# Kernel optimization log

Measured on AMD Instinct MI355X. Metric: run time of the kernel, lower is better.

The kernel has to match this reference:

```python
import jax, jax.numpy as jnp
import numpy as np

N = 512      # HiPPO state size
L = 65536    # sequence length
DT = 1e-3    # discretization step
UNROLL = 32  # scan unroll (source uses 128; 32 keeps CPU compile fast, same math)


def _make_hippo(n_state):
    # HiPPO-LegS continuous-time (A, B), as in make_hippo
    n = np.arange(n_state)
    P = np.sqrt(1 + 2 * n)
    A = P[:, None] * P[None, :]
    A = np.tril(A) - np.diag(n)
    B = np.sqrt(2 * n + 1.0)[:, None]
    return -A, B


def _discretize(A, B, step):
    # Bilinear (Tustin) discretization, as in discretize
    I = np.eye(A.shape[0])
    BL = np.linalg.inv(I - step / 2 * A)
    Ab = BL @ (I + step / 2 * A)
    Bb = (BL * step) @ B
    return Ab, Bb


def setup_inputs() -> dict:
    key = jax.random.key(0)
    A, B = _make_hippo(N)            # float64 numpy for stable inverse
    Ab, Bb = _discretize(A, B, DT)
    u = jax.random.normal(key, (L,), dtype=jnp.float32)
    return {
        "u": u,
        "Ab": jnp.asarray(Ab, dtype=jnp.float32),   # [N, N]
        "Bb": jnp.asarray(Bb, dtype=jnp.float32),   # [N, 1]
        "x0": jnp.zeros((N,), dtype=jnp.float32),   # last_x initial state
    }


def reference(u, Ab, Bb, x0):
    # Faithful HiPPO.encode: x_{k+1} = Ab @ x_k + Bb @ u_k, returning the
    # full state trajectory f of shape [L, N] (the scan's stacked outputs).
    b = Bb[:, 0]  # Bb @ u[k, None] == b * u_k

    def step(x, u_k):
        x1 = Ab @ x + b * u_k
        return x1, x1

    _, f = jax.lax.scan(step, x0, u, unroll=UNROLL)
    return f
```

## Files before the change

### kernel.cpp

```cpp
#include <hip/hip_runtime.h>
#include <cstdint>
#include <cstddef>


typedef _Float16 half_t;
typedef _Float16 f16x8 __attribute__((ext_vector_type(8)));
typedef float f32x4 __attribute__((ext_vector_type(4)));

static constexpr int KPAD = 544;
static constexpr size_t MSZ = (size_t)512 * 512;
static constexpr float INV2048 = 1.f / 2048.f;

__device__ inline void split1(float v, half_t& h, half_t& l) {
  h = (half_t)v;
  l = (half_t)((v - (float)h) * 2048.f);
}
__device__ inline void split1r(float v, half_t& h, half_t& l) {
  h = (half_t)v;
  l = (half_t)(v - (float)h);
}

__global__ void init_kernel(float4* __restrict__ zp, const float* __restrict__ Ab,
                            float* __restrict__ V0, const float* __restrict__ x0,
                            half_t* __restrict__ xh) {
  int bid = blockIdx.x, tid = threadIdx.x;
  if (bid < 6656) {
    zp[bid * 256 + tid] = make_float4(0.f, 0.f, 0.f, 0.f);
  } else if (bid < 7680) {
    int i = (bid - 6656) * 256 + tid;
    V0[i] = Ab[i];
  } else {
    xh[tid] = (half_t)x0[tid];
    xh[tid + 256] = (half_t)x0[tid + 256];
  }
}

__global__ void kbuild_kernel(const float* __restrict__ V, const float* __restrict__ b,
                              float* __restrict__ K) {
  int gw = blockIdx.x * 4 + (threadIdx.x >> 6);
  int lane = threadIdx.x & 63;
  int t = gw >> 9, n = gw & 511;
  if (t == 0) { if (lane == 0) K[n] = b[n]; return; }
  const float* row = V + (size_t)(t - 1) * MSZ + (size_t)n * 512;
  float acc = 0.f;
#pragma unroll
  for (int m = 0; m < 512; m += 64) acc += row[m + lane] * b[m + lane];
#pragma unroll
  for (int s = 32; s; s >>= 1) acc += __shfl_down(acc, s, 64);
  if (lane == 0) K[t * 512 + n] = acc;
}

__global__ void wcat_fill_kernel(const float* __restrict__ V, const float* __restrict__ K,
                                 half_t* __restrict__ Wh, half_t* __restrict__ Wl) {
  size_t idx = (size_t)blockIdx.x * 256 + threadIdx.x;
  if (idx >= (size_t)8192 * KPAD) return;
  int row = (int)(idx / KPAD), k = (int)(idx % KPAD);
  int i = row >> 9, n = row & 511;
  float v = 0.f;
  if (k < 512) v = V[(size_t)i * MSZ + (size_t)n * 512 + k];
  else if (k < 528) { int j = k - 512; if (j <= i) v = K[(i - j) * 512 + n]; }
  half_t h, l; split1r(v, h, l);
  Wh[idx] = h; Wl[idx] = l;
}

__global__ void leaf_kernel(const float* __restrict__ u, const float* __restrict__ K,
                            half_t* __restrict__ Z) {
  __shared__ float us[16];
  int c = blockIdx.x, n = threadIdx.x;
  if (n < 16) us[n] = u[c * 16 + n];
  __syncthreads();
  float acc = 0.f;
#pragma unroll
  for (int j = 0; j < 16; ++j) acc += K[(15 - j) * 512 + n] * us[j];
  Z[(size_t)c * 512 + n] = (half_t)acc;
}

__global__ void xtail_kernel(const float* __restrict__ u,
                             half_t* __restrict__ Xh, half_t* __restrict__ Xl) {
  int idx = blockIdx.x * 256 + threadIdx.x;
  int c = idx >> 5, j = idx & 31;
  float v = (j < 16) ? u[c * 16 + j] : 0.f;
  size_t o = (size_t)c * KPAD + 512 + j;
  half_t h, l; split1r(v, h, l);
  Xh[o] = h; Xl[o] = l;
}

__device__ __forceinline__ void sq_body(
    const float* __restrict__ A, const float* __restrict__ B, float* __restrict__ C,
    int bx, int by, int sl,
    half_t* __restrict__ Ash, half_t* __restrict__ Asl,
    half_t* __restrict__ Bsh, half_t* __restrict__ Bsl) {
  int m0 = bx * 64, n0 = by * 64;
  int tid = threadIdx.x, wave = tid >> 6, lane = tid & 63;
  int wm = (wave & 1) * 32, wn = (wave >> 1) * 32;
  f32x4 acc[2][2], accc[2][2];
#pragma unroll
  for (int i = 0; i < 2; ++i)
#pragma unroll
    for (int j = 0; j < 2; ++j) {
      acc[i][j] = (f32x4){0.f, 0.f, 0.f, 0.f};
      accc[i][j] = (f32x4){0.f, 0.f, 0.f, 0.f};
    }
  int rb = tid >> 6, mm = tid & 15, kseg = (tid >> 4) & 3;
  const float* ar = A + (size_t)(m0 + rb * 16 + mm) * 512 + sl * 128 + kseg * 8;
  const float* bc = B + (size_t)(sl * 128 + kseg * 8) * 512 + n0 + rb * 16 + mm;
  float4 a0 = *(const float4*)ar, a1 = *(const float4*)(ar + 4);
  float bv[8];
#pragma unroll
  for (int j = 0; j < 8; ++j) bv[j] = bc[(size_t)j * 512];
#pragma unroll
  for (int kt = 0; kt < 4; ++kt) {
    {
      float aa[8] = {a0.x, a0.y, a0.z, a0.w, a1.x, a1.y, a1.z, a1.w};
      f16x8 hv, lv;
#pragma unroll
      for (int j = 0; j < 8; ++j) { half_t h, l; split1(aa[j], h, l); hv[j] = h; lv[j] = l; }
      *(f16x8*)(Ash + tid * 8) = hv;
      *(f16x8*)(Asl + tid * 8) = lv;
#pragma unroll
      for (int j = 0; j < 8; ++j) { half_t h, l; split1(bv[j], h, l); hv[j] = h; lv[j] = l; }
      *(f16x8*)(Bsh + tid * 8) = hv;
      *(f16x8*)(Bsl + tid * 8) = lv;
    }
    __syncthreads();
    if (kt < 3) {
      a0 = *(const float4*)(ar + (kt + 1) * 32);
      a1 = *(const float4*)(ar + (kt + 1) * 32 + 4);
#pragma unroll
      for (int j = 0; j < 8; ++j) bv[j] = bc[(size_t)((kt + 1) * 32 + j) * 512];
    }
    f16x8 afh[2], afl[2], bfh[2], bfl[2];
#pragma unroll
    for (int i = 0; i < 2; ++i) {
      int ra = (wm >> 4) + i, rbn = (wn >> 4) + i;
      afh[i] = *(const f16x8*)(Ash + ra * 512 + lane * 8);
      afl[i] = *(const f16x8*)(Asl + ra * 512 + lane * 8);
      bfh[i] = *(const f16x8*)(Bsh + rbn * 512 + lane * 8);
      bfl[i] = *(const f16x8*)(Bsl + rbn * 512 + lane * 8);
    }
#pragma unroll
    for (int i = 0; i < 2; ++i)
#pragma unroll
      for (int j = 0; j < 2; ++j) {
        acc[i][j] = __builtin_amdgcn_mfma_f32_16x16x32_f16(afh[i], bfh[j], acc[i][j], 0, 0, 0);
        accc[i][j] = __builtin_amdgcn_mfma_f32_16x16x32_f16(afh[i], bfl[j], accc[i][j], 0, 0, 0);
        accc[i][j] = __builtin_amdgcn_mfma_f32_16x16x32_f16(afl[i], bfh[j], accc[i][j], 0, 0, 0);
      }
    __syncthreads();
  }
  int ml = lane & 15, quad = lane >> 4;
  for (int i = 0; i < 2; ++i)
    for (int j = 0; j < 2; ++j)
      for (int rr = 0; rr < 4; ++rr) {
        int gm = m0 + wm + i * 16 + quad * 4 + rr;
        int gn = n0 + wn + j * 16 + ml;
        atomicAdd(&C[(size_t)gm * 512 + gn], acc[i][j][rr] + accc[i][j][rr] * INV2048);
      }
}

__global__ __launch_bounds__(256)
void gemm_nn512(const float* __restrict__ A, long sA,
                const float* __restrict__ B, long sB,
                float* __restrict__ C, long sC) {
  __shared__ __align__(16) half_t s0[64 * 32], s1[64 * 32], s2[64 * 32], s3[64 * 32];
  int bz = blockIdx.z, bb = bz >> 2, sl = bz & 3;
  sq_body(A + (size_t)bb * sA, B + (size_t)bb * sB, C + (size_t)bb * sC,
          blockIdx.x, blockIdx.y, sl, s0, s1, s2, s3);
}

__device__ __forceinline__ void sweep_body(
    const half_t* __restrict__ A, long ldA, const float* __restrict__ BT,
    const half_t* __restrict__ D, long ldD,
    half_t* __restrict__ Ch, half_t* __restrict__ Cl, long ldC,
    int rScale, int rOff, int doCopy, int M, int bx, int by,
    half_t* __restrict__ Ash, half_t* __restrict__ Bsh, half_t* __restrict__ Bsl) {
  int m0 = bx * 64, n0 = by * 64;
  int tid = threadIdx.x, wave = tid >> 6, lane = tid & 63;
  int wm = (wave & 1) * 32, wn = (wave >> 1) * 32;
  f32x4 acc[2][2], accc[2][2];
#pragma unroll
  for (int i = 0; i < 2; ++i)
#pragma unroll
    for (int j = 0; j < 2; ++j) {
      acc[i][j] = (f32x4){0.f, 0.f, 0.f, 0.f};
      accc[i][j] = (f32x4){0.f, 0.f, 0.f, 0.f};
    }
  int rb = tid >> 6, mm = tid & 15, kseg = (tid >> 4) & 3;
  int arow = m0 + rb * 16 + mm;
  const half_t* ap = A + (size_t)arow * ldA + kseg * 8;
  const float* bp = BT + (size_t)(n0 + rb * 16 + mm) * 512 + kseg * 8;
  f16x8 av = (f16x8){0, 0, 0, 0, 0, 0, 0, 0};
  if (arow < M) av = *(const f16x8*)ap;
  float4 bv0 = *(const float4*)bp;
  float4 bv1 = *(const float4*)(bp + 4);
#pragma unroll
  for (int kt = 0; kt < 16; ++kt) {
    int k0 = kt * 32;
    *(f16x8*)(Ash + tid * 8) = av;
    if (doCopy && k0 >= n0 && k0 < n0 + 64 && arow < M) {
      size_t co = (size_t)(2 * arow) * ldC + k0 + kseg * 8;
      *(f16x8*)(Ch + co) = av;
      if (Cl) *(f16x8*)(Cl + co) = (f16x8){0, 0, 0, 0, 0, 0, 0, 0};
    }
    {
      float bb[8] = {bv0.x, bv0.y, bv0.z, bv0.w, bv1.x, bv1.y, bv1.z, bv1.w};
      f16x8 hv, lv;
#pragma unroll
      for (int j = 0; j < 8; ++j) { half_t h, l; split1(bb[j], h, l); hv[j] = h; lv[j] = l; }
      *(f16x8*)(Bsh + tid * 8) = hv;
      *(f16x8*)(Bsl + tid * 8) = lv;
    }
    __syncthreads();
    if (kt < 15) {
      if (arow < M) av = *(const f16x8*)(ap + (kt + 1) * 32);
      bv0 = *(const float4*)(bp + (kt + 1) * 32);
      bv1 = *(const float4*)(bp + (kt + 1) * 32 + 4);
    }
    f16x8 af[2], bfh[2], bfl[2];
#pragma unroll
    for (int i = 0; i < 2; ++i) {
      af[i] = *(const f16x8*)(Ash + ((wm >> 4) + i) * 512 + lane * 8);
      bfh[i] = *(const f16x8*)(Bsh + ((wn >> 4) + i) * 512 + lane * 8);
      bfl[i] = *(const f16x8*)(Bsl + ((wn >> 4) + i) * 512 + lane * 8);
    }
#pragma unroll
    for (int i = 0; i < 2; ++i)
#pragma unroll
      for (int j = 0; j < 2; ++j) {
        acc[i][j] = __builtin_amdgcn_mfma_f32_16x16x32_f16(af[i], bfh[j], acc[i][j], 0, 0, 0);
        accc[i][j] = __builtin_amdgcn_mfma_f32_16x16x32_f16(af[i], bfl[j], accc[i][j], 0, 0, 0);
      }
    __syncthreads();
  }
  int ml = lane & 15, quad = lane >> 4;
  for (int i = 0; i < 2; ++i)
    for (int j = 0; j < 2; ++j)
      for (int rr = 0; rr < 4; ++rr) {
        int gm = m0 + wm + i * 16 + quad * 4 + rr;
        int gn = n0 + wn + j * 16 + ml;
        if (gm >= M) continue;
        float v = acc[i][j][rr] + accc[i][j][rr] * INV2048;
        if (D) v += (float)D[(size_t)gm * ldD + gn];
        size_t co = ((size_t)gm * rScale + rOff) * ldC + gn;
        if (Cl) { half_t h, l; split1r(v, h, l); Ch[co] = h; Cl[co] = l; }
        else Ch[co] = (half_t)v;
      }
}

__global__ __launch_bounds__(256)
void gemm_nt_sweep(const half_t* __restrict__ A, long ldA,
                   const float* __restrict__ BT,
                   const half_t* __restrict__ D, long ldD,
                   half_t* __restrict__ Ch, half_t* __restrict__ Cl,
                   long ldC, int rScale, int rOff, int doCopy, int M) {
  __shared__ __align__(16) half_t s0[64 * 32], s1[64 * 32], s2[64 * 32];
  sweep_body(A, ldA, BT, D, ldD, Ch, Cl, ldC, rScale, rOff, doCopy, M,
             blockIdx.x, blockIdx.y, s0, s1, s2);
}

__global__ __launch_bounds__(256)
void fused_up(const float* __restrict__ T, float* __restrict__ Tout,
              const half_t* __restrict__ Zin, half_t* __restrict__ Zout, int M) {
  __shared__ __align__(16) half_t s0[64 * 32], s1[64 * 32], s2[64 * 32], s3[64 * 32];
  int bid = blockIdx.x;
  if (bid < 256) {
    sq_body(T, T, Tout, bid & 7, (bid >> 3) & 7, bid >> 6, s0, s1, s2, s3);
  } else {
    int b = bid - 256;
    sweep_body(Zin, 1024L, T, Zin + 512, 1024L, Zout, (half_t*)0, 512L,
               1, 0, 0, M, b >> 3, b & 7, s0, s1, s2);
  }
}

__device__ inline void load_lds16(const half_t* g, half_t* l) {
  __builtin_amdgcn_global_load_lds(
      (const __attribute__((address_space(1))) uint32_t*)g,
      (__attribute__((address_space(3))) uint32_t*)l, 16, 0, 0);
}

__global__ __launch_bounds__(512, 2)
void gemm_main(const half_t* __restrict__ Ah, const half_t* __restrict__ Al,
               const half_t* __restrict__ Bh, const half_t* __restrict__ Bl,
               float* __restrict__ C) {
  __shared__ __align__(16) half_t sm[2 * 4 * 8192];
  int bid = blockIdx.x;
  int xcd = bid & 7, loc = bid >> 3;
  int mt = (xcd & 1) * 8 + (loc >> 3);
  int nt = (xcd >> 1) * 8 + (loc & 7);
  int m0 = mt * 256, n0 = nt * 256;
  int tid = threadIdx.x, wave = tid >> 6, lane = tid & 63;
  int wm = (wave & 1) * 128, wn = (wave >> 1) * 64;
  int mm = lane & 15, kseg = lane >> 4;
  f32x4 acc[8][4];
#pragma unroll
  for (int f = 0; f < 8; ++f)
#pragma unroll
    for (int g = 0; g < 4; ++g) acc[f][g] = (f32x4){0.f, 0.f, 0.f, 0.f};

  const size_t ga0 = (size_t)(m0 + wave * 16 + mm) * KPAD + kseg * 8;
  const size_t gb0 = (size_t)(n0 + wave * 16 + mm) * KPAD + kseg * 8;
  const size_t qstep = (size_t)128 * KPAD;

  auto stage = [&](int nb, int kt, int q) {
    size_t go = (size_t)kt * 32 + (size_t)q * qstep;
    half_t* d = sm + (size_t)nb * 32768 + (size_t)(wave + 8 * q) * 512;
    load_lds16(Ah + ga0 + go, d);
    load_lds16(Al + ga0 + go, d + 8192);
    load_lds16(Bh + gb0 + go, d + 16384);
    load_lds16(Bl + gb0 + go, d + 24576);
  };

  stage(0, 0, 0);
  stage(0, 0, 1);
  asm volatile("s_waitcnt vmcnt(0)" ::: "memory");
  __builtin_amdgcn_s_barrier();

  const int lread = lane * 8;
  const int arow = (wm >> 4);
  const int brow = (wn >> 4);
  for (int kt = 0; kt < 17; ++kt) {
    const int cur = kt & 1;
    const half_t* SA_h = sm + cur * 32768;
    const half_t* SA_l = SA_h + 8192;
    const half_t* SB_h = SA_h + 16384;
    const half_t* SB_l = SA_h + 24576;
    const bool pre = kt < 16;
    f16x8 ah[4], al[4], bh0[2], bl0[2], bh1[2], bl1[2];

#pragma unroll
    for (int i = 0; i < 4; ++i) {
      ah[i] = *(const f16x8*)(SA_h + (arow + i) * 512 + lread);
      al[i] = *(const f16x8*)(SA_l + (arow + i) * 512 + lread);
    }
#pragma unroll
    for (int j = 0; j < 2; ++j) {
      bh0[j] = *(const f16x8*)(SB_h + (brow + j) * 512 + lread);
      bl0[j] = *(const f16x8*)(SB_l + (brow + j) * 512 + lread);
    }
    if (pre) stage(cur ^ 1, kt + 1, 0);
    __builtin_amdgcn_s_barrier();
    asm volatile("s_waitcnt lgkmcnt(0)" ::: "memory");
    __builtin_amdgcn_sched_barrier(0);
    __builtin_amdgcn_s_setprio(1);
#pragma unroll
    for (int i = 0; i < 4; ++i)
#pragma unroll
      for (int j = 0; j < 2; ++j) {
        acc[i][j] = __builtin_amdgcn_mfma_f32_16x16x32_f16(ah[i], bh0[j], acc[i][j], 0, 0, 0);
        acc[i][j] = __builtin_amdgcn_mfma_f32_16x16x32_f16(ah[i], bl0[j], acc[i][j], 0, 0, 0);
        acc[i][j] = __builtin_amdgcn_mfma_f32_16x16x32_f16(al[i], bh0[j], acc[i][j], 0, 0, 0);
      }
    __builtin_amdgcn_s_setprio(0);
    __builtin_amdgcn_s_barrier();

#pragma unroll
    for (int j = 0; j < 2; ++j) {
      bh1[j] = *(const f16x8*)(SB_h + (brow + 2 + j) * 512 + lread);
      bl1[j] = *(const f16x8*)(SB_l + (brow + 2 + j) * 512 + lread);
    }
    if (pre) stage(cur ^ 1, kt + 1, 1);
    __builtin_amdgcn_s_barrier();
    asm volatile("s_waitcnt lgkmcnt(0)" ::: "memory");
    __builtin_amdgcn_sched_barrier(0);
    __builtin_amdgcn_s_setprio(1);
#pragma unroll
    for (int i = 0; i < 4; ++i)
#pragma unroll
      for (int j = 0; j < 2; ++j) {
        acc[i][2 + j] = __builtin_amdgcn_mfma_f32_16x16x32_f16(ah[i], bh1[j], acc[i][2 + j], 0, 0, 0);
        acc[i][2 + j] = __builtin_amdgcn_mfma_f32_16x16x32_f16(ah[i], bl1[j], acc[i][2 + j], 0, 0, 0);
        acc[i][2 + j] = __builtin_amdgcn_mfma_f32_16x16x32_f16(al[i], bh1[j], acc[i][2 + j], 0, 0, 0);
      }
    __builtin_amdgcn_s_setprio(0);
    __builtin_amdgcn_s_barrier();

#pragma unroll
    for (int i = 0; i < 4; ++i) {
      ah[i] = *(const f16x8*)(SA_h + (arow + 4 + i) * 512 + lread);
      al[i] = *(const f16x8*)(SA_l + (arow + 4 + i) * 512 + lread);
    }
    __builtin_amdgcn_s_barrier();
    asm volatile("s_waitcnt lgkmcnt(0)" ::: "memory");
    __builtin_amdgcn_sched_barrier(0);
    __builtin_amdgcn_s_setprio(1);
#pragma unroll
    for (int i = 0; i < 4; ++i)
#pragma unroll
      for (int j = 0; j < 2; ++j) {
        acc[4 + i][2 + j] = __builtin_amdgcn_mfma_f32_16x16x32_f16(ah[i], bh1[j], acc[4 + i][2 + j], 0, 0, 0);
        acc[4 + i][2 + j] = __builtin_amdgcn_mfma_f32_16x16x32_f16(ah[i], bl1[j], acc[4 + i][2 + j], 0, 0, 0);
        acc[4 + i][2 + j] = __builtin_amdgcn_mfma_f32_16x16x32_f16(al[i], bh1[j], acc[4 + i][2 + j], 0, 0, 0);
      }
#pragma unroll
    for (int i = 0; i < 4; ++i)
#pragma unroll
      for (int j = 0; j < 2; ++j) {
        acc[4 + i][j] = __builtin_amdgcn_mfma_f32_16x16x32_f16(ah[i], bh0[j], acc[4 + i][j], 0, 0, 0);
        acc[4 + i][j] = __builtin_amdgcn_mfma_f32_16x16x32_f16(ah[i], bl0[j], acc[4 + i][j], 0, 0, 0);
        acc[4 + i][j] = __builtin_amdgcn_mfma_f32_16x16x32_f16(al[i], bh0[j], acc[4 + i][j], 0, 0, 0);
      }
    __builtin_amdgcn_s_setprio(0);
    asm volatile("s_waitcnt vmcnt(0)" ::: "memory");
    __builtin_amdgcn_s_barrier();
  }

  int ml = lane & 15, quad = lane >> 4;
#pragma unroll
  for (int f = 0; f < 8; ++f)
#pragma unroll
    for (int g = 0; g < 4; ++g) {
      int gm = m0 + wm + f * 16 + quad * 4;
      int gn = n0 + wn + g * 16 + ml;
      float* o = C + (size_t)gm * 8192 + gn;
#pragma unroll
      for (int rr = 0; rr < 4; ++rr)
        o[(size_t)rr * 8192] = acc[f][g][rr];
    }
}


extern "C" void kernel_launch(void* const* d_in, const int* in_sizes, int n_in,
                              void* d_out, int out_size, void* d_ws, size_t ws_size,
                              hipStream_t stream) {
  (void)in_sizes; (void)n_in; (void)out_size; (void)ws_size;
  const float* u  = (const float*)d_in[0];
  const float* Ab = (const float*)d_in[1];
  const float* Bb = (const float*)d_in[2];
  const float* x0 = (const float*)d_in[3];
  float* out = (float*)d_out;

  char* base = (char*)d_ws;
  size_t off = 0;
  auto carve = [&](size_t bytes) -> char* {
    char* p = base + off;
    off = (off + bytes + 255) & ~(size_t)255;
    return p;
  };
  float*  Vp  = (float*)carve(16 * MSZ * 4);
  float*  Sp  = (float*)carve(11 * MSZ * 4);
  float*  Kb  = (float*)carve((size_t)16 * 512 * 4);
  half_t* Wh  = (half_t*)carve((size_t)8192 * KPAD * 2);
  half_t* Wl  = (half_t*)carve((size_t)8192 * KPAD * 2);
  half_t* x0h = (half_t*)carve(512 * 2);
  size_t zoff[13]; zoff[0] = 0;
  for (int l = 0; l < 12; ++l) zoff[l + 1] = zoff[l] + (size_t)(4096 >> l) * 512;
  size_t xoff[13]; xoff[1] = 0;
  for (int l = 1; l < 12; ++l) xoff[l + 1] = xoff[l] + (size_t)(4096 >> l) * 512;
  half_t* Zh  = (half_t*)Vp;
  half_t* Xph = (half_t*)((char*)Vp + ((zoff[12] * 2 + 255) & ~(size_t)255));
  half_t* Xch = (half_t*)Sp;
  half_t* Xcl = (half_t*)((char*)Sp + (((size_t)4096 * KPAD * 2 + 255) & ~(size_t)255));

  hipLaunchKernelGGL(init_kernel, dim3(7681), dim3(256), 0, stream,
                     (float4*)(Vp + MSZ), Ab, Vp, x0, x0h);

  for (int s = 1; s <= 8; s <<= 1) {
    hipLaunchKernelGGL(gemm_nn512, dim3(8, 8, 4 * s), dim3(256), 0, stream,
                       Vp, (long)MSZ,
                       Vp + (size_t)(s - 1) * MSZ, 0L,
                       Vp + (size_t)s * MSZ, (long)MSZ);
  }

  hipLaunchKernelGGL(kbuild_kernel, dim3(2048), dim3(256), 0, stream, Vp, Bb, Kb);
  hipLaunchKernelGGL(wcat_fill_kernel,
                     dim3((unsigned)(((size_t)8192 * KPAD + 255) / 256)), dim3(256), 0, stream,
                     Vp, Kb, Wh, Wl);
  hipLaunchKernelGGL(leaf_kernel, dim3(4096), dim3(512), 0, stream, u, Kb, Zh);

  auto Smat = [&](int l) -> const float* {
    return (l == 0) ? (Vp + 15 * MSZ) : (Sp + (size_t)(l - 1) * MSZ);
  };

  for (int l = 1; l <= 11; ++l) {
    const float* T = (l == 1) ? Vp + 15 * MSZ : Sp + (size_t)(l - 2) * MSZ;
    float* Tout = Sp + (size_t)(l - 1) * MSZ;
    int Mup = 1 << (12 - l);
    int nswp = ((Mup + 63) / 64) * 8;
    hipLaunchKernelGGL(fused_up, dim3(256 + nswp), dim3(256), 0, stream,
                       T, Tout, Zh + zoff[l - 1], Zh + zoff[l], Mup);
  }

  for (int l = 11; l >= 0; --l) {
    int M = 1 << (11 - l);
    const half_t* Xup = (l == 11) ? x0h : Xph + xoff[l + 1];
    half_t* Ch = (l == 0) ? Xch : Xph + xoff[l];
    half_t* Cl = (l == 0) ? Xcl : (half_t*)0;
    long ldC = (l == 0) ? (long)KPAD : 512L;
    if (l == 0) {
      hipLaunchKernelGGL(xtail_kernel, dim3(512), dim3(256), 0, stream, u, Xch, Xcl);
    }
    hipLaunchKernelGGL(gemm_nt_sweep, dim3((unsigned)((M + 63) / 64), 8), dim3(256), 0, stream,
                       Xup, 512L, Smat(l),
                       Zh + zoff[l], 1024L,
                       Ch, Cl, ldC, 2, 1, 1, M);
  }

  hipLaunchKernelGGL(gemm_main, dim3(512), dim3(512), 0, stream, Xch, Xcl, Wh, Wl, out);
}
```

Baseline: 699.0 us.

## Pair down-sweep levels with precomputed product matrices to halve launches

Replaces the twelve serial down-sweep launches with six paired launches. Each launch computes two tree levels directly from the grandparent state, using a precomputed product matrix P of two adjacent level transition matrices and a precomputed Y-Z correction term. A prep kernel builds the first P and the Y-Z terms and copies one S matrix. Each pair launch also computes the next P, and the final launch absorbs the xtail work. The wcat fill is vectorised to eight elements per thread. The aim is to shorten the serial chain of small latency-bound launches. In exchange the code does extra GEMM work for the P products and has more complex indexing.

```diff
diff --git a/kernel.cpp b/kernel.cpp
--- a/kernel.cpp
+++ b/kernel.cpp
@@ -19,6 +19,166 @@
   h = (half_t)v;
   l = (half_t)(v - (float)h);
 }
+
+template <int NKT, bool ATOM>
+__device__ __forceinline__ void sq_body(
+    const float* __restrict__ A, const float* __restrict__ B, float* __restrict__ C,
+    int bx, int by, int k0off,
+    half_t* __restrict__ Ash, half_t* __restrict__ Asl,
+    half_t* __restrict__ Bsh, half_t* __restrict__ Bsl) {
+  int m0 = bx * 64, n0 = by * 64;
+  int tid = threadIdx.x, wave = tid >> 6, lane = tid & 63;
+  int wm = (wave & 1) * 32, wn = (wave >> 1) * 32;
+  f32x4 acc[2][2], accc[2][2];
+#pragma unroll
+  for (int i = 0; i < 2; ++i)
+#pragma unroll
+    for (int j = 0; j < 2; ++j) {
+      acc[i][j] = (f32x4){0.f, 0.f, 0.f, 0.f};
+      accc[i][j] = (f32x4){0.f, 0.f, 0.f, 0.f};
+    }
+  int rb = tid >> 6, mm = tid & 15, kseg = (tid >> 4) & 3;
+  const float* ar = A + (size_t)(m0 + rb * 16 + mm) * 512 + k0off + kseg * 8;
+  const float* bc = B + (size_t)(k0off + kseg * 8) * 512 + n0 + rb * 16 + mm;
+  float4 a0 = *(const float4*)ar, a1 = *(const float4*)(ar + 4);
+  float bv[8];
+#pragma unroll
+  for (int j = 0; j < 8; ++j) bv[j] = bc[(size_t)j * 512];
+#pragma unroll
+  for (int kt = 0; kt < NKT; ++kt) {
+    {
+      float aa[8] = {a0.x, a0.y, a0.z, a0.w, a1.x, a1.y, a1.z, a1.w};
+      f16x8 hv, lv;
+#pragma unroll
+      for (int j = 0; j < 8; ++j) { half_t h, l; split1(aa[j], h, l); hv[j] = h; lv[j] = l; }
+      *(f16x8*)(Ash + tid * 8) = hv;
+      *(f16x8*)(Asl + tid * 8) = lv;
+#pragma unroll
+      for (int j = 0; j < 8; ++j) { half_t h, l; split1(bv[j], h, l); hv[j] = h; lv[j] = l; }
+      *(f16x8*)(Bsh + tid * 8) = hv;
+      *(f16x8*)(Bsl + tid * 8) = lv;
+    }
+    __syncthreads();
+    if (kt < NKT - 1) {
+      a0 = *(const float4*)(ar + (kt + 1) * 32);
+      a1 = *(const float4*)(ar + (kt + 1) * 32 + 4);
+#pragma unroll
+      for (int j = 0; j < 8; ++j) bv[j] = bc[(size_t)((kt + 1) * 32 + j) * 512];
+    }
+    f16x8 afh[2], afl[2], bfh[2], bfl[2];
+#pragma unroll
+    for (int i = 0; i < 2; ++i) {
+      int ra = (wm >> 4) + i, rbn = (wn >> 4) + i;
+      afh[i] = *(const f16x8*)(Ash + ra * 512 + lane * 8);
+      afl[i] = *(const f16x8*)(Asl + ra * 512 + lane * 8);
+      bfh[i] = *(const f16x8*)(Bsh + rbn * 512 + lane * 8);
+      bfl[i] = *(const f16x8*)(Bsl + rbn * 512 + lane * 8);
+    }
+#pragma unroll
+    for (int i = 0; i < 2; ++i)
+#pragma unroll
+      for (int j = 0; j < 2; ++j) {
+        acc[i][j] = __builtin_amdgcn_mfma_f32_16x16x32_f16(afh[i], bfh[j], acc[i][j], 0, 0, 0);
+        accc[i][j] = __builtin_amdgcn_mfma_f32_16x16x32_f16(afh[i], bfl[j], accc[i][j], 0, 0, 0);
+        accc[i][j] = __builtin_amdgcn_mfma_f32_16x16x32_f16(afl[i], bfh[j], accc[i][j], 0, 0, 0);
+      }
+    __syncthreads();
+  }
+  int ml = lane & 15, quad = lane >> 4;
+  for (int i = 0; i < 2; ++i)
+    for (int j = 0; j < 2; ++j)
+      for (int rr = 0; rr < 4; ++rr) {
+        int gm = m0 + wm + i * 16 + quad * 4 + rr;
+        int gn = n0 + wn + j * 16 + ml;
+        float v = acc[i][j][rr] + accc[i][j][rr] * INV2048;
+        if (ATOM) atomicAdd(&C[(size_t)gm * 512 + gn], v);
+        else C[(size_t)gm * 512 + gn] = v;
+      }
+}
+
+__device__ __forceinline__ void sweep_body(
+    const half_t* __restrict__ A, long ldA, const float* __restrict__ BT,
+    const half_t* __restrict__ D, long ldD,
+    half_t* __restrict__ Ch, half_t* __restrict__ Cl, long ldC,
+    int rScale, int rOff, int doCopy, int M, int bx, int by,
+    half_t* __restrict__ Ash, half_t* __restrict__ Bsh, half_t* __restrict__ Bsl) {
+  int m0 = bx * 64, n0 = by * 64;
+  int tid = threadIdx.x, wave = tid >> 6, lane = tid & 63;
+  int wm = (wave & 1) * 32, wn = (wave >> 1) * 32;
+  f32x4 acc[2][2], accc[2][2];
+#pragma unroll
+  for (int i = 0; i < 2; ++i)
+#pragma unroll
+    for (int j = 0; j < 2; ++j) {
+      acc[i][j] = (f32x4){0.f, 0.f, 0.f, 0.f};
+      accc[i][j] = (f32x4){0.f, 0.f, 0.f, 0.f};
+    }
+  int rb = tid >> 6, mm = tid & 15, kseg = (tid >> 4) & 3;
+  int arow = m0 + rb * 16 + mm;
+  const half_t* ap = A + (size_t)arow * ldA + kseg * 8;
+  const float* bp = BT + (size_t)(n0 + rb * 16 + mm) * 512 + kseg * 8;
+  f16x8 av = (f16x8){0, 0, 0, 0, 0, 0, 0, 0};
+  if (arow < M) av = *(const f16x8*)ap;
+  float4 bv0 = *(const float4*)bp;
+  float4 bv1 = *(const float4*)(bp + 4);
+#pragma unroll
+  for (int kt = 0; kt < 16; ++kt) {
+    int k0 = kt * 32;
+    *(f16x8*)(Ash + tid * 8) = av;
+    if (doCopy && k0 >= n0 && k0 < n0 + 64 && arow < M) {
+      size_t co = (size_t)rScale * arow * ldC + k0 + kseg * 8;
+      *(f16x8*)(Ch + co) = av;
+      if (Cl) *(f16x8*)(Cl + co) = (f16x8){0, 0, 0, 0, 0, 0, 0, 0};
+    }
+    {
+      float bb[8] = {bv0.x, bv0.y, bv0.z, bv0.w, bv1.x, bv1.y, bv1.z, bv1.w};
+      f16x8 hv, lv;
+#pragma unroll
+      for (int j = 0; j < 8; ++j) { half_t h, l; split1(bb[j], h, l); hv[j] = h; lv[j] = l; }
+      *(f16x8*)(Bsh + tid * 8) = hv;
+      *(f16x8*)(Bsl + tid * 8) = lv;
+    }
+    __syncthreads();
+    if (kt < 15) {
+      if (arow < M) av = *(const f16x8*)(ap + (kt + 1) * 32);
+      bv0 = *(const float4*)(bp + (kt + 1) * 32);
+      bv1 = *(const float4*)(bp + (kt + 1) * 32 + 4);
+    }
+    f16x8 af[2], bfh[2], bfl[2];
+#pragma unroll
+    for (int i = 0; i < 2; ++i) {
+      af[i] = *(const f16x8*)(Ash + ((wm >> 4) + i) * 512 + lane * 8);
+      bfh[i] = *(const f16x8*)(Bsh + ((wn >> 4) + i) * 512 + lane * 8);
+      bfl[i] = *(const f16x8*)(Bsl + ((wn >> 4) + i) * 512 + lane * 8);
+    }
+#pragma unroll
+    for (int i = 0; i < 2; ++i)
+#pragma unroll
+      for (int j = 0; j < 2; ++j) {
+        acc[i][j] = __builtin_amdgcn_mfma_f32_16x16x32_f16(af[i], bfh[j], acc[i][j], 0, 0, 0);
+        accc[i][j] = __builtin_amdgcn_mfma_f32_16x16x32_f16(af[i], bfl[j], accc[i][j], 0, 0, 0);
+      }
+    __syncthreads();
+  }
+  int ml = lane & 15, quad = lane >> 4;
+  for (int i = 0; i < 2; ++i)
+    for (int j = 0; j < 2; ++j)
+      for (int rr = 0; rr < 4; ++rr) {
+        int gm = m0 + wm + i * 16 + quad * 4 + rr;
+        int gn = n0 + wn + j * 16 + ml;
+        if (gm >= M) continue;
+        float v = acc[i][j][rr] + accc[i][j][rr] * INV2048;
+        if (D) v += (float)D[(size_t)gm * ldD + gn];
+        size_t co = ((size_t)gm * rScale + rOff) * ldC + gn;
+        if (Cl) { half_t h, l; split1r(v, h, l); Ch[co] = h; Cl[co] = l; }
+        else Ch[co] = (half_t)v;
+      }
+}
+
+__device__ __forceinline__ size_t zoff_f(int l) {
+  return ((size_t)1 << 22) - ((size_t)1 << (22 - l));
+}
+
 
 __global__ void init_kernel(float4* __restrict__ zp, const float* __restrict__ Ab,
                             float* __restrict__ V0, const float* __restrict__ x0,
@@ -52,15 +212,29 @@
 
 __global__ void wcat_fill_kernel(const float* __restrict__ V, const float* __restrict__ K,
                                  half_t* __restrict__ Wh, half_t* __restrict__ Wl) {
-  size_t idx = (size_t)blockIdx.x * 256 + threadIdx.x;
-  if (idx >= (size_t)8192 * KPAD) return;
-  int row = (int)(idx / KPAD), k = (int)(idx % KPAD);
+  int un = blockIdx.x * 256 + threadIdx.x;
+  if (un >= 8192 * 68) return;
+  int row = un / 68, kb = un - row * 68;
   int i = row >> 9, n = row & 511;
-  float v = 0.f;
-  if (k < 512) v = V[(size_t)i * MSZ + (size_t)n * 512 + k];
-  else if (k < 528) { int j = k - 512; if (j <= i) v = K[(i - j) * 512 + n]; }
-  half_t h, l; split1r(v, h, l);
-  Wh[idx] = h; Wl[idx] = l;
+  f16x8 hv, lv;
+  if (kb < 64) {
+    const float* vp = V + (size_t)i * MSZ + (size_t)n * 512 + kb * 8;
+    float4 v0 = *(const float4*)vp, v1 = *(const float4*)(vp + 4);
+    float vv[8] = {v0.x, v0.y, v0.z, v0.w, v1.x, v1.y, v1.z, v1.w};
+#pragma unroll
+    for (int j = 0; j < 8; ++j) { half_t h, l; split1r(vv[j], h, l); hv[j] = h; lv[j] = l; }
+  } else {
+#pragma unroll
+    for (int j = 0; j < 8; ++j) {
+      int k = kb * 8 + j;
+      float v = 0.f;
+      if (k < 528) { int jj = k - 512; if (jj <= i) v = K[(i - jj) * 512 + n]; }
+      half_t h, l; split1r(v, h, l); hv[j] = h; lv[j] = l;
+    }
+  }
+  size_t o = (size_t)row * KPAD + kb * 8;
+  *(f16x8*)(Wh + o) = hv;
+  *(f16x8*)(Wl + o) = lv;
 }
 
 __global__ void leaf_kernel(const float* __restrict__ u, const float* __restrict__ K,
@@ -75,187 +249,14 @@
   Z[(size_t)c * 512 + n] = (half_t)acc;
 }
 
-__global__ void xtail_kernel(const float* __restrict__ u,
-                             half_t* __restrict__ Xh, half_t* __restrict__ Xl) {
-  int idx = blockIdx.x * 256 + threadIdx.x;
-  int c = idx >> 5, j = idx & 31;
-  float v = (j < 16) ? u[c * 16 + j] : 0.f;
-  size_t o = (size_t)c * KPAD + 512 + j;
-  half_t h, l; split1r(v, h, l);
-  Xh[o] = h; Xl[o] = l;
-}
-
-__device__ __forceinline__ void sq_body(
-    const float* __restrict__ A, const float* __restrict__ B, float* __restrict__ C,
-    int bx, int by, int sl,
-    half_t* __restrict__ Ash, half_t* __restrict__ Asl,
-    half_t* __restrict__ Bsh, half_t* __restrict__ Bsl) {
-  int m0 = bx * 64, n0 = by * 64;
-  int tid = threadIdx.x, wave = tid >> 6, lane = tid & 63;
-  int wm = (wave & 1) * 32, wn = (wave >> 1) * 32;
-  f32x4 acc[2][2], accc[2][2];
-#pragma unroll
-  for (int i = 0; i < 2; ++i)
-#pragma unroll
-    for (int j = 0; j < 2; ++j) {
-      acc[i][j] = (f32x4){0.f, 0.f, 0.f, 0.f};
-      accc[i][j] = (f32x4){0.f, 0.f, 0.f, 0.f};
-    }
-  int rb = tid >> 6, mm = tid & 15, kseg = (tid >> 4) & 3;
-  const float* ar = A + (size_t)(m0 + rb * 16 + mm) * 512 + sl * 128 + kseg * 8;
-  const float* bc = B + (size_t)(sl * 128 + kseg * 8) * 512 + n0 + rb * 16 + mm;
-  float4 a0 = *(const float4*)ar, a1 = *(const float4*)(ar + 4);
-  float bv[8];
-#pragma unroll
-  for (int j = 0; j < 8; ++j) bv[j] = bc[(size_t)j * 512];
-#pragma unroll
-  for (int kt = 0; kt < 4; ++kt) {
-    {
-      float aa[8] = {a0.x, a0.y, a0.z, a0.w, a1.x, a1.y, a1.z, a1.w};
-      f16x8 hv, lv;
-#pragma unroll
-      for (int j = 0; j < 8; ++j) { half_t h, l; split1(aa[j], h, l); hv[j] = h; lv[j] = l; }
-      *(f16x8*)(Ash + tid * 8) = hv;
-      *(f16x8*)(Asl + tid * 8) = lv;
-#pragma unroll
-      for (int j = 0; j < 8; ++j) { half_t h, l; split1(bv[j], h, l); hv[j] = h; lv[j] = l; }
-      *(f16x8*)(Bsh + tid * 8) = hv;
-      *(f16x8*)(Bsl + tid * 8) = lv;
-    }
-    __syncthreads();
-    if (kt < 3) {
-      a0 = *(const float4*)(ar + (kt + 1) * 32);
-      a1 = *(const float4*)(ar + (kt + 1) * 32 + 4);
-#pragma unroll
-      for (int j = 0; j < 8; ++j) bv[j] = bc[(size_t)((kt + 1) * 32 + j) * 512];
-    }
-    f16x8 afh[2], afl[2], bfh[2], bfl[2];
-#pragma unroll
-    for (int i = 0; i < 2; ++i) {
-      int ra = (wm >> 4) + i, rbn = (wn >> 4) + i;
-      afh[i] = *(const f16x8*)(Ash + ra * 512 + lane * 8);
-      afl[i] = *(const f16x8*)(Asl + ra * 512 + lane * 8);
-      bfh[i] = *(const f16x8*)(Bsh + rbn * 512 + lane * 8);
-      bfl[i] = *(const f16x8*)(Bsl + rbn * 512 + lane * 8);
-    }
-#pragma unroll
-    for (int i = 0; i < 2; ++i)
-#pragma unroll
-      for (int j = 0; j < 2; ++j) {
-        acc[i][j] = __builtin_amdgcn_mfma_f32_16x16x32_f16(afh[i], bfh[j], acc[i][j], 0, 0, 0);
-        accc[i][j] = __builtin_amdgcn_mfma_f32_16x16x32_f16(afh[i], bfl[j], accc[i][j], 0, 0, 0);
-        accc[i][j] = __builtin_amdgcn_mfma_f32_16x16x32_f16(afl[i], bfh[j], accc[i][j], 0, 0, 0);
-      }
-    __syncthreads();
-  }
-  int ml = lane & 15, quad = lane >> 4;
-  for (int i = 0; i < 2; ++i)
-    for (int j = 0; j < 2; ++j)
-      for (int rr = 0; rr < 4; ++rr) {
-        int gm = m0 + wm + i * 16 + quad * 4 + rr;
-        int gn = n0 + wn + j * 16 + ml;
-        atomicAdd(&C[(size_t)gm * 512 + gn], acc[i][j][rr] + accc[i][j][rr] * INV2048);
-      }
-}
-
 __global__ __launch_bounds__(256)
 void gemm_nn512(const float* __restrict__ A, long sA,
                 const float* __restrict__ B, long sB,
                 float* __restrict__ C, long sC) {
   __shared__ __align__(16) half_t s0[64 * 32], s1[64 * 32], s2[64 * 32], s3[64 * 32];
   int bz = blockIdx.z, bb = bz >> 2, sl = bz & 3;
-  sq_body(A + (size_t)bb * sA, B + (size_t)bb * sB, C + (size_t)bb * sC,
-          blockIdx.x, blockIdx.y, sl, s0, s1, s2, s3);
-}
-
-__device__ __forceinline__ void sweep_body(
-    const half_t* __restrict__ A, long ldA, const float* __restrict__ BT,
-    const half_t* __restrict__ D, long ldD,
-    half_t* __restrict__ Ch, half_t* __restrict__ Cl, long ldC,
-    int rScale, int rOff, int doCopy, int M, int bx, int by,
-    half_t* __restrict__ Ash, half_t* __restrict__ Bsh, half_t* __restrict__ Bsl) {
-  int m0 = bx * 64, n0 = by * 64;
-  int tid = threadIdx.x, wave = tid >> 6, lane = tid & 63;
-  int wm = (wave & 1) * 32, wn = (wave >> 1) * 32;
-  f32x4 acc[2][2], accc[2][2];
-#pragma unroll
-  for (int i = 0; i < 2; ++i)
-#pragma unroll
-    for (int j = 0; j < 2; ++j) {
-      acc[i][j] = (f32x4){0.f, 0.f, 0.f, 0.f};
-      accc[i][j] = (f32x4){0.f, 0.f, 0.f, 0.f};
-    }
-  int rb = tid >> 6, mm = tid & 15, kseg = (tid >> 4) & 3;
-  int arow = m0 + rb * 16 + mm;
-  const half_t* ap = A + (size_t)arow * ldA + kseg * 8;
-  const float* bp = BT + (size_t)(n0 + rb * 16 + mm) * 512 + kseg * 8;
-  f16x8 av = (f16x8){0, 0, 0, 0, 0, 0, 0, 0};
-  if (arow < M) av = *(const f16x8*)ap;
-  float4 bv0 = *(const float4*)bp;
-  float4 bv1 = *(const float4*)(bp + 4);
-#pragma unroll
-  for (int kt = 0; kt < 16; ++kt) {
-    int k0 = kt * 32;
-    *(f16x8*)(Ash + tid * 8) = av;
-    if (doCopy && k0 >= n0 && k0 < n0 + 64 && arow < M) {
-      size_t co = (size_t)(2 * arow) * ldC + k0 + kseg * 8;
-      *(f16x8*)(Ch + co) = av;
-      if (Cl) *(f16x8*)(Cl + co) = (f16x8){0, 0, 0, 0, 0, 0, 0, 0};
-    }
-    {
-      float bb[8] = {bv0.x, bv0.y, bv0.z, bv0.w, bv1.x, bv1.y, bv1.z, bv1.w};
-      f16x8 hv, lv;
-#pragma unroll
-      for (int j = 0; j < 8; ++j) { half_t h, l; split1(bb[j], h, l); hv[j] = h; lv[j] = l; }
-      *(f16x8*)(Bsh + tid * 8) = hv;
-      *(f16x8*)(Bsl + tid * 8) = lv;
-    }
-    __syncthreads();
-    if (kt < 15) {
-      if (arow < M) av = *(const f16x8*)(ap + (kt + 1) * 32);
-      bv0 = *(const float4*)(bp + (kt + 1) * 32);
-      bv1 = *(const float4*)(bp + (kt + 1) * 32 + 4);
-    }
-    f16x8 af[2], bfh[2], bfl[2];
-#pragma unroll
-    for (int i = 0; i < 2; ++i) {
-      af[i] = *(const f16x8*)(Ash + ((wm >> 4) + i) * 512 + lane * 8);
-      bfh[i] = *(const f16x8*)(Bsh + ((wn >> 4) + i) * 512 + lane * 8);
-      bfl[i] = *(const f16x8*)(Bsl + ((wn >> 4) + i) * 512 + lane * 8);
-    }
-#pragma unroll
-    for (int i = 0; i < 2; ++i)
-#pragma unroll
-      for (int j = 0; j < 2; ++j) {
-        acc[i][j] = __builtin_amdgcn_mfma_f32_16x16x32_f16(af[i], bfh[j], acc[i][j], 0, 0, 0);
-        accc[i][j] = __builtin_amdgcn_mfma_f32_16x16x32_f16(af[i], bfl[j], accc[i][j], 0, 0, 0);
-      }
-    __syncthreads();
-  }
-  int ml = lane & 15, quad = lane >> 4;
-  for (int i = 0; i < 2; ++i)
-    for (int j = 0; j < 2; ++j)
-      for (int rr = 0; rr < 4; ++rr) {
-        int gm = m0 + wm + i * 16 + quad * 4 + rr;
-        int gn = n0 + wn + j * 16 + ml;
-        if (gm >= M) continue;
-        float v = acc[i][j][rr] + accc[i][j][rr] * INV2048;
-        if (D) v += (float)D[(size_t)gm * ldD + gn];
-        size_t co = ((size_t)gm * rScale + rOff) * ldC + gn;
-        if (Cl) { half_t h, l; split1r(v, h, l); Ch[co] = h; Cl[co] = l; }
-        else Ch[co] = (half_t)v;
-      }
-}
-
-__global__ __launch_bounds__(256)
-void gemm_nt_sweep(const half_t* __restrict__ A, long ldA,
-                   const float* __restrict__ BT,
-                   const half_t* __restrict__ D, long ldD,
-                   half_t* __restrict__ Ch, half_t* __restrict__ Cl,
-                   long ldC, int rScale, int rOff, int doCopy, int M) {
-  __shared__ __align__(16) half_t s0[64 * 32], s1[64 * 32], s2[64 * 32];
-  sweep_body(A, ldA, BT, D, ldD, Ch, Cl, ldC, rScale, rOff, doCopy, M,
-             blockIdx.x, blockIdx.y, s0, s1, s2);
+  sq_body<4, true>(A + (size_t)bb * sA, B + (size_t)bb * sB, C + (size_t)bb * sC,
+                   blockIdx.x, blockIdx.y, sl * 128, s0, s1, s2, s3);
 }
 
 __global__ __launch_bounds__(256)
@@ -264,12 +265,77 @@
   __shared__ __align__(16) half_t s0[64 * 32], s1[64 * 32], s2[64 * 32], s3[64 * 32];
   int bid = blockIdx.x;
   if (bid < 256) {
-    sq_body(T, T, Tout, bid & 7, (bid >> 3) & 7, bid >> 6, s0, s1, s2, s3);
+    sq_body<4, true>(T, T, Tout, bid & 7, (bid >> 3) & 7, (bid >> 6) * 128, s0, s1, s2, s3);
   } else {
     int b = bid - 256;
     sweep_body(Zin, 1024L, T, Zin + 512, 1024L, Zout, (half_t*)0, 512L,
                1, 0, 0, M, b >> 3, b & 7, s0, s1, s2);
   }
+}
+
+__global__ __launch_bounds__(256)
+void prep_kernel(const float* __restrict__ Vp, const float* __restrict__ Sp,
+                 const half_t* __restrict__ Zh, half_t* __restrict__ YZp,
+                 float* __restrict__ P10, float* __restrict__ S1c) {
+  __shared__ __align__(16) half_t s0[64 * 32], s1[64 * 32], s2[64 * 32], s3[64 * 32];
+  int bid = blockIdx.x, tid = threadIdx.x;
+  if (bid < 64) {
+    sq_body<16, false>(Sp + (size_t)9 * MSZ, Sp + (size_t)10 * MSZ, P10,
+                       bid & 7, bid >> 3, 0, s0, s1, s2, s3);
+    return;
+  }
+  int yb = bid - 64;
+  const int yzr[6] = {0, 1, 5, 21, 85, 341};
+#pragma unroll
+  for (int t = 0; t < 6; ++t) {
+    int l = 10 - 2 * t;
+    int M0 = 1 << (2 * t);
+    int nb = ((M0 + 63) >> 6) * 8;
+    if (yb < nb) {
+      const float* Sl = (l == 0) ? Vp + 15 * MSZ : Sp + (size_t)(l - 1) * MSZ;
+      sweep_body(Zh + zoff_f(l + 1), 1024L, Sl,
+                 Zh + zoff_f(l) + 1024, 2048L,
+                 YZp + (size_t)yzr[t] * 512, (half_t*)0, 512L,
+                 1, 0, 0, M0, yb >> 3, yb & 7, s0, s1, s2);
+      return;
+    }
+    yb -= nb;
+  }
+  ((float4*)S1c)[(size_t)yb * 256 + tid] = ((const float4*)Sp)[(size_t)yb * 256 + tid];
+}
+
+__global__ __launch_bounds__(256)
+void down_pair(const half_t* __restrict__ Xin, int M0,
+               const float* __restrict__ Sl, const float* __restrict__ Sl1,
+               const float* __restrict__ Pl,
+               const half_t* __restrict__ Zl, const half_t* __restrict__ Zl1,
+               const half_t* __restrict__ YZ,
+               half_t* __restrict__ Ch, half_t* __restrict__ Cl, long ldC,
+               const float* __restrict__ Pna, const float* __restrict__ Pnb,
+               float* __restrict__ Pnout, const float* __restrict__ uu) {
+  __shared__ __align__(16) half_t s0[64 * 32], s1[64 * 32], s2[64 * 32], s3[64 * 32];
+  int bid = blockIdx.x, tid = threadIdx.x;
+  int nrole = ((M0 + 63) >> 6) * 8;
+  if (bid < 3 * nrole) {
+    int r = bid / nrole, b = bid - r * nrole;
+    const float* BT = (r == 0) ? Sl : (r == 1) ? Sl1 : Pl;
+    const half_t* D = (r == 0) ? Zl : (r == 1) ? Zl1 : YZ;
+    long ldD = (r == 0) ? 2048L : (r == 1) ? 1024L : 512L;
+    sweep_body(Xin, 512L, BT, D, ldD, Ch, Cl, ldC,
+               4, r + 1, (r == 0) ? 1 : 0, M0, b >> 3, b & 7, s0, s1, s2);
+    return;
+  }
+  int rest = bid - 3 * nrole;
+  if (Pnout) {
+    sq_body<16, false>(Pna, Pnb, Pnout, rest & 7, rest >> 3, 0, s0, s1, s2, s3);
+    return;
+  }
+  int idx = rest * 256 + tid;
+  int c = idx >> 5, j = idx & 31;
+  float v = (j < 16) ? uu[c * 16 + j] : 0.f;
+  size_t o = (size_t)c * KPAD + 512 + j;
+  half_t h, l; split1r(v, h, l);
+  Ch[o] = h; Cl[o] = l;
 }
 
 __device__ inline void load_lds16(const half_t* g, half_t* l) {
@@ -442,12 +508,19 @@
   half_t* Wh  = (half_t*)carve((size_t)8192 * KPAD * 2);
   half_t* Wl  = (half_t*)carve((size_t)8192 * KPAD * 2);
   half_t* x0h = (half_t*)carve(512 * 2);
+  float*  Pp  = (float*)carve(3 * MSZ * 4);
+  float*  Pb0 = Pp;
+  float*  Pb1 = Pp + MSZ;
+  float*  S1c = Pp + 2 * MSZ;
+
   size_t zoff[13]; zoff[0] = 0;
   for (int l = 0; l < 12; ++l) zoff[l + 1] = zoff[l] + (size_t)(4096 >> l) * 512;
   size_t xoff[13]; xoff[1] = 0;
   for (int l = 1; l < 12; ++l) xoff[l + 1] = xoff[l] + (size_t)(4096 >> l) * 512;
   half_t* Zh  = (half_t*)Vp;
-  half_t* Xph = (half_t*)((char*)Vp + ((zoff[12] * 2 + 255) & ~(size_t)255));
+  size_t xphOff = (zoff[12] * 2 + 255) & ~(size_t)255;
+  half_t* Xph = (half_t*)((char*)Vp + xphOff);
+  half_t* YZp = (half_t*)((char*)Vp + xphOff + ((xoff[12] * 2 + 255) & ~(size_t)255));
   half_t* Xch = (half_t*)Sp;
   half_t* Xcl = (half_t*)((char*)Sp + (((size_t)4096 * KPAD * 2 + 255) & ~(size_t)255));
 
@@ -460,11 +533,8 @@
                        Vp + (size_t)(s - 1) * MSZ, 0L,
                        Vp + (size_t)s * MSZ, (long)MSZ);
   }
-
   hipLaunchKernelGGL(kbuild_kernel, dim3(2048), dim3(256), 0, stream, Vp, Bb, Kb);
-  hipLaunchKernelGGL(wcat_fill_kernel,
-                     dim3((unsigned)(((size_t)8192 * KPAD + 255) / 256)), dim3(256), 0, stream,
-                     Vp, Kb, Wh, Wl);
+  hipLaunchKernelGGL(wcat_fill_kernel, dim3(2176), dim3(256), 0, stream, Vp, Kb, Wh, Wl);
   hipLaunchKernelGGL(leaf_kernel, dim3(4096), dim3(512), 0, stream, u, Kb, Zh);
 
   auto Smat = [&](int l) -> const float* {
@@ -472,7 +542,7 @@
   };
 
   for (int l = 1; l <= 11; ++l) {
-    const float* T = (l == 1) ? Vp + 15 * MSZ : Sp + (size_t)(l - 2) * MSZ;
+    const float* T = Smat(l - 1);
     float* Tout = Sp + (size_t)(l - 1) * MSZ;
     int Mup = 1 << (12 - l);
     int nswp = ((Mup + 63) / 64) * 8;
@@ -480,19 +550,31 @@
                        T, Tout, Zh + zoff[l - 1], Zh + zoff[l], Mup);
   }
 
-  for (int l = 11; l >= 0; --l) {
-    int M = 1 << (11 - l);
-    const half_t* Xup = (l == 11) ? x0h : Xph + xoff[l + 1];
-    half_t* Ch = (l == 0) ? Xch : Xph + xoff[l];
-    half_t* Cl = (l == 0) ? Xcl : (half_t*)0;
-    long ldC = (l == 0) ? (long)KPAD : 512L;
-    if (l == 0) {
-      hipLaunchKernelGGL(xtail_kernel, dim3(512), dim3(256), 0, stream, u, Xch, Xcl);
-    }
-    hipLaunchKernelGGL(gemm_nt_sweep, dim3((unsigned)((M + 63) / 64), 8), dim3(256), 0, stream,
-                       Xup, 512L, Smat(l),
-                       Zh + zoff[l], 1024L,
-                       Ch, Cl, ldC, 2, 1, 1, M);
+  hipLaunchKernelGGL(prep_kernel, dim3(512), dim3(256), 0, stream,
+                     Vp, Sp, Zh, YZp, Pb0, S1c);
+
+  const int yzrow[6] = {0, 1, 5, 21, 85, 341};
+  for (int i = 0; i < 6; ++i) {
+    int l = 10 - 2 * i;
+    int M0 = 1 << (2 * i);
+    const float* Sl  = Smat(l);
+    const float* Sl1 = (i == 5) ? S1c : Smat(l + 1);
+    const float* Pl  = (i & 1) ? Pb1 : Pb0;
+    const float* Pna = (i < 5) ? Smat(l - 2) : (const float*)0;
+    const float* Pnb = (i < 5) ? Smat(l - 1) : (const float*)0;
+    float* Pnout     = (i < 5) ? ((i & 1) ? Pb0 : Pb1) : (float*)0;
+    const half_t* Xin = (i == 0) ? x0h : Xph + xoff[l + 2];
+    half_t* Ch = (i == 5) ? Xch : Xph + xoff[l];
+    half_t* Cl = (i == 5) ? Xcl : (half_t*)0;
+    long ldC = (i == 5) ? (long)KPAD : 512L;
+    const float* uu = (i == 5) ? u : (const float*)0;
+    int nrole = ((M0 + 63) / 64) * 8;
+    int grid = 3 * nrole + (i < 5 ? 64 : 0) + (i == 5 ? 512 : 0);
+    hipLaunchKernelGGL(down_pair, dim3(grid), dim3(256), 0, stream,
+                       Xin, M0, Sl, Sl1, Pl,
+                       Zh + zoff[l], Zh + zoff[l + 1],
+                       YZp + (size_t)yzrow[i] * 512,
+                       Ch, Cl, ldC, Pna, Pnb, Pnout, uu);
   }
 
   hipLaunchKernelGGL(gemm_main, dim3(512), dim3(512), 0, stream, Xch, Xcl, Wh, Wl, out);
```

Result: faster. 642.2 us (-8.1%).
